# Performance work log

Measured on AMD Instinct MI355X. Metric: run time of the kernel, lower is better.

## Reference

```python
import jax, jax.numpy as jnp
import numpy as np
from jax import lax

B, C, H, W = 16, 512, 32, 32
CQ = C // 16


def _conv(x, w, b):
    # NCHW input, OIHW kernel, 3x3 stride-1 'SAME' == torch padding=1
    o = lax.conv_general_dilated(x, w, (1, 1), 'SAME',
                                 dimension_numbers=('NCHW', 'OIHW', 'NCHW'))
    return o + b[None, :, None, None]


def setup_inputs() -> dict:
    key = jax.random.key(0)
    ks = jax.random.split(key, 8)
    fan_q = C * 9
    fan_v = C * 9
    return {
        'x': jax.random.normal(ks[0], (B, C, H, W), jnp.float32),
        'y': jax.random.normal(ks[1], (B, C, H, W), jnp.float32),
        'wq': jax.random.normal(ks[2], (CQ, C, 3, 3), jnp.float32) / np.sqrt(fan_q),
        'bq': jnp.zeros((CQ,), jnp.float32),
        'wk': jax.random.normal(ks[3], (CQ, C, 3, 3), jnp.float32) / np.sqrt(fan_q),
        'bk': jnp.zeros((CQ,), jnp.float32),
        'wv': jax.random.normal(ks[4], (C, C, 3, 3), jnp.float32) / np.sqrt(fan_v),
        'bv': jnp.zeros((C,), jnp.float32),
    }


def reference(x, y, wq, bq, wk, bk, wv, bv):
    b, c, h, w = x.shape
    n = h * w
    q = _conv(x, wq, bq).reshape(b, -1, n)   # (B, CQ, N)
    k = _conv(y, wk, bk).reshape(b, -1, n)   # (B, CQ, N)
    v = _conv(y, wv, bv).reshape(b, c, n)    # (B, C, N)
    # energy[b, i, j] = <q[:, i], k[:, j]>  (unscaled, non-causal)
    energy = jnp.einsum('bdi,bdj->bij', q, k)           # (B, N, N)
    attn = jax.nn.softmax(energy, axis=-1)              # softmax over keys j
    # out[b, c, i] = sum_j v[b, c, j] * attn[b, i, j]
    out = jnp.einsum('bcj,bij->bci', v, attn)           # (B, C, N)
    return out.reshape(b, c, h, w)
```

## Files before the change

kernel.cpp:

```cpp
#include <hip/hip_runtime.h>

#define BB 16
#define CCH 512
#define CQD 32
#define HH 32
#define WW 32
#define NN 1024
#define PH 34

typedef __attribute__((ext_vector_type(8))) _Float16 half8;
typedef __attribute__((ext_vector_type(4))) _Float16 half4;
typedef __attribute__((ext_vector_type(4))) float f32x4;

static __device__ __forceinline__ void gload_lds16(const void* g, void* l) {
    __builtin_amdgcn_global_load_lds(
        (const __attribute__((address_space(1))) unsigned int*)g,
        (__attribute__((address_space(3))) unsigned int*)l, 16, 0, 0);
}

__global__ __launch_bounds__(256) void prep_all_kernel(
    const float* __restrict__ x, const float* __restrict__ y,
    const float* __restrict__ wv, const float* __restrict__ wq,
    const float* __restrict__ wk,
    _Float16* __restrict__ xp, _Float16* __restrict__ yp,
    _Float16* __restrict__ wvh, _Float16* __restrict__ wqkh)
{
    const int bid = blockIdx.x;
    const int t = threadIdx.x;

    if (bid >= 1088) {
        const int wb = bid - 1088;
        const float* src;
        _Float16* dst;
        int co_src, co_dst;
        if (wb < 512)      { src = wv; co_src = wb;       dst = wvh;  co_dst = wb; }
        else if (wb < 544) { src = wq; co_src = wb - 512; dst = wqkh; co_dst = wb - 512; }
        else               { src = wk; co_src = wb - 544; dst = wqkh; co_dst = 32 + (wb - 544); }
        for (int idx = t; idx < 4608; idx += 256) {
            int tap = idx / 512, ci = idx - tap * 512;
            dst[(size_t)co_dst * 4608 + idx] = (_Float16)src[(size_t)co_src * 4608 + ci * 9 + tap];
        }
        return;
    }

    const int h = bid >> 5;
    const int which = (bid >> 4) & 1, b = bid & 15;
    const float* img = which ? y : x;
    _Float16* row = (which ? yp : xp) + (size_t)(b * PH + h) * PH * CCH;
    const int gh = h - 1;

    half8 z;
    #pragma unroll
    for (int u = 0; u < 8; ++u) z[u] = (_Float16)0.f;

    if (gh < 0 || gh >= HH) {
        for (int idx = t; idx < PH * CCH / 8; idx += 256)
            *(half8*)&row[(size_t)idx * 8] = z;
        return;
    }

    __shared__ float X[64][33];
    for (int ci0 = 0; ci0 < CCH; ci0 += 64) {
        __syncthreads();
        #pragma unroll
        for (int i = 0; i < 8; ++i) {
            int ci = i * 8 + (t >> 5), w = t & 31;
            X[ci][w] = img[((size_t)(b * CCH + ci0 + ci) * HH + gh) * WW + w];
        }
        __syncthreads();
        int w = t >> 3, g = t & 7;
        half8 o;
        #pragma unroll
        for (int u = 0; u < 8; ++u) o[u] = (_Float16)X[g * 8 + u][w];
        *(half8*)&row[(size_t)(w + 1) * CCH + ci0 + g * 8] = o;
        if (t < 16) {
            int col = (t < 8) ? 0 : 33;
            *(half8*)&row[(size_t)col * CCH + ci0 + (t & 7) * 8] = z;
        }
    }
}

__global__ __launch_bounds__(256, 2) void conv_v_mfma_kernel(
    const _Float16* __restrict__ yp,
    const _Float16* __restrict__ wvh,
    const float* __restrict__ bvb,
    _Float16* __restrict__ vout)
{
    const int pt  = blockIdx.x;
    const int co0 = blockIdx.y * 64;
    const int b   = blockIdx.z;

    __shared__ __align__(16) _Float16 Wl[64 * 296];
    __shared__ __align__(16) _Float16 Yl[13824];

    const int t    = threadIdx.x;
    const int lane = t & 63;
    const int wv4  = t >> 6;
    const int l15  = lane & 15;
    const int kg   = lane >> 4;

    f32x4 acc[4][4];
    #pragma unroll
    for (int m = 0; m < 4; ++m)
        #pragma unroll
        for (int n = 0; n < 4; ++n) {
            f32x4 z = {0.f, 0.f, 0.f, 0.f};
            acc[m][n] = z;
        }

    const int r0p = pt * 8;
    int bbase[4];
    #pragma unroll
    for (int n = 0; n < 4; ++n) {
        int pxl = wv4 * 64 + n * 16 + l15;
        int rl = pxl >> 5, cl = pxl & 31;
        bbase[n] = (rl * 34 + cl) * 40 + kg * 8;
    }
    int abase[4];
    #pragma unroll
    for (int m = 0; m < 4; ++m)
        abase[m] = (m * 16 + l15) * 296 + kg * 8;

    #pragma unroll 1
    for (int ci0 = 0; ci0 < CCH; ci0 += 32) {
        __syncthreads();
        #pragma unroll
        for (int i = 0; i < 10; ++i) {
            int d = t + i * 256;
            if (d < 2368) {
                int c = d / 37, rem = d - c * 37;
                const _Float16* g = (rem < 36)
                    ? &wvh[(size_t)(co0 + c) * 4608 + (rem >> 2) * 512 + ci0 + (rem & 3) * 8]
                    : wvh;
                gload_lds16(g, (char*)Wl + (size_t)(i * 256 + wv4 * 64) * 16);
            }
        }
        #pragma unroll
        for (int i = 0; i < 7; ++i) {
            int d = t + i * 256;
            if (d < 1728) {
                int rc = d / 5, part = d - rc * 5;
                const _Float16* g = yp;
                if (rc < 340 && part < 4) {
                    int r = rc / 34, c = rc - r * 34;
                    g = &yp[((size_t)(b * PH + r0p + r) * PH + c) * CCH + ci0 + part * 8];
                }
                gload_lds16(g, (char*)Yl + (size_t)(i * 256 + wv4 * 64) * 16);
            }
        }
        __syncthreads();

        #pragma unroll
        for (int tap = 0; tap < 9; ++tap) {
            const int dh = tap / 3, dw = tap % 3;
            half8 a[4], bf[4];
            #pragma unroll
            for (int m = 0; m < 4; ++m)
                a[m] = *(const half8*)&Wl[abase[m] + tap * 32];
            #pragma unroll
            for (int n = 0; n < 4; ++n)
                bf[n] = *(const half8*)&Yl[bbase[n] + (dh * 34 + dw) * 40];
            #pragma unroll
            for (int m = 0; m < 4; ++m)
                #pragma unroll
                for (int n = 0; n < 4; ++n)
                    acc[m][n] = __builtin_amdgcn_mfma_f32_16x16x32_f16(a[m], bf[n], acc[m][n], 0, 0, 0);
        }
    }

    #pragma unroll
    for (int m = 0; m < 4; ++m) {
        #pragma unroll
        for (int reg = 0; reg < 4; ++reg) {
            int co = co0 + m * 16 + kg * 4 + reg;
            float bias = bvb[co];
            #pragma unroll
            for (int n = 0; n < 4; ++n) {
                int px = pt * 256 + wv4 * 64 + n * 16 + l15;
                vout[((size_t)b * CCH + co) * NN + px] = (_Float16)(acc[m][n][reg] + bias);
            }
        }
    }
}

__global__ __launch_bounds__(256, 4) void conv_qk_split_kernel(
    const _Float16* __restrict__ xp,
    const _Float16* __restrict__ yp,
    const _Float16* __restrict__ wqkh,
    float* __restrict__ pbuf)
{
    const int pt    = blockIdx.x >> 2;
    const int ks    = blockIdx.x & 3;
    const int which = blockIdx.y;
    const int b     = blockIdx.z;
    const _Float16* in = which ? yp : xp;

    __shared__ __align__(16) _Float16 Wl[9728];
    __shared__ __align__(16) _Float16 Xl[8192];

    const int t    = threadIdx.x;
    const int lane = t & 63;
    const int w    = t >> 6;
    const int l15  = lane & 15;
    const int kg   = lane >> 4;

    f32x4 acc[2][2];
    #pragma unroll
    for (int m = 0; m < 2; ++m)
        #pragma unroll
        for (int n = 0; n < 2; ++n) {
            f32x4 z = {0.f, 0.f, 0.f, 0.f};
            acc[m][n] = z;
        }

    const int r0p = pt * 4;
    int bbase[2];
    #pragma unroll
    for (int n = 0; n < 2; ++n) {
        int pxl = w * 32 + n * 16 + l15;
        int rl = pxl >> 5, cl = pxl & 31;
        bbase[n] = (rl * 34 + cl) * 40 + kg * 8;
    }
    int abase[2];
    #pragma unroll
    for (int m = 0; m < 2; ++m)
        abase[m] = (m * 16 + l15) * 296 + kg * 8;

    #pragma unroll 1
    for (int cc = 0; cc < 4; ++cc) {
        const int ci0 = ks * 128 + cc * 32;
        __syncthreads();
        #pragma unroll
        for (int i = 0; i < 5; ++i) {
            int d = t + i * 256;
            if (d < 1216) {
                const _Float16* g = wqkh;
                if (d < 1184) {
                    int c = d / 37, rem = d - c * 37;
                    if (rem < 36)
                        g = &wqkh[(size_t)(which * 32 + c) * 4608 + (rem >> 2) * 512 + ci0 + (rem & 3) * 8];
                }
                gload_lds16(g, (char*)Wl + (size_t)(i * 256 + w * 64) * 16);
            }
        }
        #pragma unroll
        for (int i = 0; i < 4; ++i) {
            int d = t + i * 256;
            int rc = d / 5, part = d - rc * 5;
            const _Float16* g = in;
            if (rc < 204 && part < 4) {
                int r = rc / 34, c = rc - r * 34;
                g = &in[((size_t)(b * PH + r0p + r) * PH + c) * CCH + ci0 + part * 8];
            }
            gload_lds16(g, (char*)Xl + (size_t)(i * 256 + w * 64) * 16);
        }
        __syncthreads();

        #pragma unroll
        for (int tap = 0; tap < 9; ++tap) {
            const int dh = tap / 3, dw = tap % 3;
            half8 a[2], bfr[2];
            #pragma unroll
            for (int m = 0; m < 2; ++m)
                a[m] = *(const half8*)&Wl[abase[m] + tap * 32];
            #pragma unroll
            for (int n = 0; n < 2; ++n)
                bfr[n] = *(const half8*)&Xl[bbase[n] + (dh * 34 + dw) * 40];
            #pragma unroll
            for (int m = 0; m < 2; ++m)
                #pragma unroll
                for (int n = 0; n < 2; ++n)
                    acc[m][n] = __builtin_amdgcn_mfma_f32_16x16x32_f16(a[m], bfr[n], acc[m][n], 0, 0, 0);
        }
    }

    float* pb = &pbuf[(((size_t)(ks * 2 + which) * BB + b) * NN) * CQD];
    #pragma unroll
    for (int n = 0; n < 2; ++n) {
        int px = pt * 128 + w * 32 + n * 16 + l15;
        #pragma unroll
        for (int m = 0; m < 2; ++m) {
            float4 o = make_float4(acc[m][n][0], acc[m][n][1], acc[m][n][2], acc[m][n][3]);
            *(float4*)&pb[(size_t)px * CQD + m * 16 + kg * 4] = o;
        }
    }
}

__global__ __launch_bounds__(256) void qk_reduce_kernel(
    const float* __restrict__ pbuf,
    const float* __restrict__ bq, const float* __restrict__ bk,
    _Float16* __restrict__ qh, _Float16* __restrict__ kh)
{
    const int gid   = blockIdx.x * 256 + threadIdx.x;
    const int cog   = gid & 7;
    const int px    = (gid >> 3) & 1023;
    const int b     = (gid >> 13) & 15;
    const int which = gid >> 17;

    const size_t base = (((size_t)which * BB + b) * NN + px) * CQD + cog * 4;
    const size_t kstep = (size_t)2 * BB * NN * CQD;
    float4 s = *(const float4*)&pbuf[base];
    #pragma unroll
    for (int ks = 1; ks < 4; ++ks) {
        float4 p = *(const float4*)&pbuf[base + ks * kstep];
        s.x += p.x; s.y += p.y; s.z += p.z; s.w += p.w;
    }
    const float* bias = which ? bk : bq;
    float4 bv = *(const float4*)&bias[cog * 4];
    half4 o;
    o[0] = (_Float16)(s.x + bv.x);
    o[1] = (_Float16)(s.y + bv.y);
    o[2] = (_Float16)(s.z + bv.z);
    o[3] = (_Float16)(s.w + bv.w);
    _Float16* out = which ? kh : qh;
    *(half4*)&out[((size_t)b * NN + px) * CQD + cog * 4] = o;
}

__global__ __launch_bounds__(256, 2) void attn_fused_kernel(
    const _Float16* __restrict__ qh,
    const _Float16* __restrict__ kh,
    const _Float16* __restrict__ v,
    float* __restrict__ out)
{
    const int wg   = blockIdx.x;
    const int virt = (wg & 7) * 64 + (wg >> 3);
    const int b    = virt >> 5;
    const int i0   = (virt & 31) * 32;

    __shared__ __align__(16) _Float16 Pl[32 * 136];
    float* redm = (float*)Pl;
    float* redl = redm + 32 * 17;

    const int t    = threadIdx.x;
    const int lane = t & 63;
    const int w    = t >> 6;
    const int l15  = lane & 15;
    const int kg   = lane >> 4;

    half8 qb[2];
    #pragma unroll
    for (int n = 0; n < 2; ++n)
        qb[n] = *(const half8*)&qh[((size_t)b * NN + i0 + n * 16 + l15) * CQD + kg * 8];

    float m[2] = {-3.0e38f, -3.0e38f}, l[2] = {0.f, 0.f};
    #pragma unroll 1
    for (int jp = 0; jp < 8; ++jp) {
        #pragma unroll
        for (int ht = 0; ht < 2; ++ht) {
            int j = jp * 128 + ht * 64 + w * 16 + l15;
            half8 ak = *(const half8*)&kh[((size_t)b * NN + j) * CQD + kg * 8];
            #pragma unroll
            for (int n = 0; n < 2; ++n) {
                f32x4 s = {0.f, 0.f, 0.f, 0.f};
                s = __builtin_amdgcn_mfma_f32_16x16x32_f16(ak, qb[n], s, 0, 0, 0);
                float tm = fmaxf(fmaxf(s[0], s[1]), fmaxf(s[2], s[3]));
                float m2 = fmaxf(m[n], tm);
                l[n] = l[n] * __expf(m[n] - m2)
                     + __expf(s[0] - m2) + __expf(s[1] - m2)
                     + __expf(s[2] - m2) + __expf(s[3] - m2);
                m[n] = m2;
            }
        }
    }
    #pragma unroll
    for (int n = 0; n < 2; ++n) {
        redm[(n * 16 + l15) * 17 + w * 4 + kg] = m[n];
        redl[(n * 16 + l15) * 17 + w * 4 + kg] = l[n];
    }
    __syncthreads();
    float mr[2], rl[2];
    #pragma unroll
    for (int n = 0; n < 2; ++n) {
        const int i = n * 16 + l15;
        float M = redm[i * 17];
        #pragma unroll
        for (int p = 1; p < 16; ++p) M = fmaxf(M, redm[i * 17 + p]);
        float L = 0.f;
        #pragma unroll
        for (int p = 0; p < 16; ++p) L += redl[i * 17 + p] * __expf(redm[i * 17 + p] - M);
        mr[n] = M;
        rl[n] = 1.f / L;
    }

    f32x4 acc[4][2][2];
    #pragma unroll
    for (int cc = 0; cc < 4; ++cc)
        #pragma unroll
        for (int mm = 0; mm < 2; ++mm)
            #pragma unroll
            for (int n = 0; n < 2; ++n) {
                f32x4 z = {0.f, 0.f, 0.f, 0.f};
                acc[cc][mm][n] = z;
            }

    #pragma unroll 1
    for (int jp = 0; jp < 8; ++jp) {
        __syncthreads();
        #pragma unroll
        for (int ht = 0; ht < 2; ++ht) {
            int j = jp * 128 + ht * 64 + w * 16 + l15;
            half8 ak = *(const half8*)&kh[((size_t)b * NN + j) * CQD + kg * 8];
            #pragma unroll
            for (int n = 0; n < 2; ++n) {
                f32x4 s = {0.f, 0.f, 0.f, 0.f};
                s = __builtin_amdgcn_mfma_f32_16x16x32_f16(ak, qb[n], s, 0, 0, 0);
                half4 p4;
                #pragma unroll
                for (int reg = 0; reg < 4; ++reg)
                    p4[reg] = (_Float16)(__expf(s[reg] - mr[n]) * rl[n]);
                *(half4*)&Pl[(n * 16 + l15) * 136 + ht * 64 + w * 16 + kg * 4] = p4;
            }
        }
        __syncthreads();
        #pragma unroll
        for (int cc = 0; cc < 4; ++cc) {
            #pragma unroll
            for (int ks = 0; ks < 4; ++ks) {
                half8 pb[2], va[2];
                #pragma unroll
                for (int n = 0; n < 2; ++n)
                    pb[n] = *(const half8*)&Pl[(n * 16 + l15) * 136 + ks * 32 + kg * 8];
                #pragma unroll
                for (int mm = 0; mm < 2; ++mm) {
                    int c = cc * 128 + w * 32 + mm * 16 + l15;
                    va[mm] = *(const half8*)&v[((size_t)b * CCH + c) * NN + jp * 128 + ks * 32 + kg * 8];
                }
                #pragma unroll
                for (int mm = 0; mm < 2; ++mm)
                    #pragma unroll
                    for (int n = 0; n < 2; ++n)
                        acc[cc][mm][n] = __builtin_amdgcn_mfma_f32_16x16x32_f16(va[mm], pb[n], acc[cc][mm][n], 0, 0, 0);
            }
        }
    }

    #pragma unroll
    for (int cc = 0; cc < 4; ++cc)
        #pragma unroll
        for (int mm = 0; mm < 2; ++mm)
            #pragma unroll
            for (int n = 0; n < 2; ++n)
                #pragma unroll
                for (int reg = 0; reg < 4; ++reg) {
                    int c = cc * 128 + w * 32 + mm * 16 + kg * 4 + reg;
                    out[((size_t)b * CCH + c) * NN + i0 + n * 16 + l15] = acc[cc][mm][n][reg];
                }
}

extern "C" void kernel_launch(void* const* d_in, const int* in_sizes, int n_in,
                              void* d_out, int out_size, void* d_ws, size_t ws_size,
                              hipStream_t stream) {
    const float* x  = (const float*)d_in[0];
    const float* y  = (const float*)d_in[1];
    const float* wq = (const float*)d_in[2];
    const float* bq = (const float*)d_in[3];
    const float* wk = (const float*)d_in[4];
    const float* bk = (const float*)d_in[5];
    const float* wv = (const float*)d_in[6];
    const float* bv = (const float*)d_in[7];
    float* out = (float*)d_out;

    _Float16* qhb = (_Float16*)d_ws;
    _Float16* khb = qhb + (size_t)BB * NN * CQD;
    _Float16* vb   = khb + (size_t)BB * NN * CQD;
    _Float16* ypb  = vb + (size_t)BB * CCH * NN;
    _Float16* xpb  = ypb + (size_t)BB * PH * PH * CCH;
    _Float16* wvh  = xpb + (size_t)BB * PH * PH * CCH;
    _Float16* wqkh = wvh + (size_t)512 * 4608;
    float* pbuf = (float*)vb;

    prep_all_kernel<<<dim3(1088 + 576), 256, 0, stream>>>(x, y, wv, wq, wk, xpb, ypb, wvh, wqkh);
    conv_qk_split_kernel<<<dim3(32, 2, BB), 256, 0, stream>>>(xpb, ypb, wqkh, pbuf);
    qk_reduce_kernel<<<dim3(1024), 256, 0, stream>>>(pbuf, bq, bk, qhb, khb);
    conv_v_mfma_kernel<<<dim3(4, 8, BB), 256, 0, stream>>>(ypb, wvh, bv, vb);
    attn_fused_kernel<<<dim3(512), 256, 0, stream>>>(qhb, khb, vb, out);
}
```

Measured before the change: 201.7 us.

## Retile attention to 64 queries x 256 channels and stage V tiles in LDS

```diff
diff --git a/kernel.cpp b/kernel.cpp
--- a/kernel.cpp
+++ b/kernel.cpp
@@ -325,11 +325,14 @@
     const int wg   = blockIdx.x;
     const int virt = (wg & 7) * 64 + (wg >> 3);
     const int b    = virt >> 5;
-    const int i0   = (virt & 31) * 32;
-
-    __shared__ __align__(16) _Float16 Pl[32 * 136];
+    const int rem5 = virt & 31;
+    const int c0   = (rem5 >> 4) * 256;
+    const int i0   = (rem5 & 15) * 64;
+
+    __shared__ __align__(16) _Float16 Vl[2][64 * 136];
+    __shared__ __align__(16) _Float16 Pl[64 * 136];
     float* redm = (float*)Pl;
-    float* redl = redm + 32 * 17;
+    float* redl = redm + 64 * 17;
 
     const int t    = threadIdx.x;
     const int lane = t & 63;
@@ -337,12 +340,28 @@
     const int l15  = lane & 15;
     const int kg   = lane >> 4;
 
-    half8 qb[2];
-    #pragma unroll
-    for (int n = 0; n < 2; ++n)
+    #define STAGE_V(dst, jp_, cc_)                                              \
+        {                                                                       \
+            _Pragma("unroll")                                                   \
+            for (int i_ = 0; i_ < 5; ++i_) {                                    \
+                int d_ = t + i_ * 256;                                          \
+                if (d_ < 1088) {                  \
+                    int r_ = d_ / 17, rem_ = d_ - r_ * 17;                      \
+                    const _Float16* g_ = (rem_ < 16)                            \
+                        ? &v[((size_t)b * CCH + c0 + (cc_) * 64 + r_) * NN + (jp_) * 128 + rem_ * 8] \
+                        : v;                                                    \
+                    gload_lds16(g_, (char*)(dst) + (size_t)(i_ * 256 + w * 64) * 16); \
+                }                                                               \
+            }                                                                   \
+        }
+
+    half8 qb[4];
+    #pragma unroll
+    for (int n = 0; n < 4; ++n)
         qb[n] = *(const half8*)&qh[((size_t)b * NN + i0 + n * 16 + l15) * CQD + kg * 8];
 
-    float m[2] = {-3.0e38f, -3.0e38f}, l[2] = {0.f, 0.f};
+    float m[4] = {-3.0e38f, -3.0e38f, -3.0e38f, -3.0e38f};
+    float l[4] = {0.f, 0.f, 0.f, 0.f};
     #pragma unroll 1
     for (int jp = 0; jp < 8; ++jp) {
         #pragma unroll
@@ -350,7 +369,7 @@
             int j = jp * 128 + ht * 64 + w * 16 + l15;
             half8 ak = *(const half8*)&kh[((size_t)b * NN + j) * CQD + kg * 8];
             #pragma unroll
-            for (int n = 0; n < 2; ++n) {
+            for (int n = 0; n < 4; ++n) {
                 f32x4 s = {0.f, 0.f, 0.f, 0.f};
                 s = __builtin_amdgcn_mfma_f32_16x16x32_f16(ak, qb[n], s, 0, 0, 0);
                 float tm = fmaxf(fmaxf(s[0], s[1]), fmaxf(s[2], s[3]));
@@ -363,14 +382,14 @@
         }
     }
     #pragma unroll
-    for (int n = 0; n < 2; ++n) {
+    for (int n = 0; n < 4; ++n) {
         redm[(n * 16 + l15) * 17 + w * 4 + kg] = m[n];
         redl[(n * 16 + l15) * 17 + w * 4 + kg] = l[n];
     }
     __syncthreads();
-    float mr[2], rl[2];
-    #pragma unroll
-    for (int n = 0; n < 2; ++n) {
+    float mr[4], rl[4];
+    #pragma unroll
+    for (int n = 0; n < 4; ++n) {
         const int i = n * 16 + l15;
         float M = redm[i * 17];
         #pragma unroll
@@ -382,26 +401,25 @@
         rl[n] = 1.f / L;
     }
 
-    f32x4 acc[4][2][2];
+    f32x4 acc[4][4];
     #pragma unroll
     for (int cc = 0; cc < 4; ++cc)
         #pragma unroll
-        for (int mm = 0; mm < 2; ++mm)
-            #pragma unroll
-            for (int n = 0; n < 2; ++n) {
-                f32x4 z = {0.f, 0.f, 0.f, 0.f};
-                acc[cc][mm][n] = z;
-            }
+        for (int n = 0; n < 4; ++n) {
+            f32x4 z = {0.f, 0.f, 0.f, 0.f};
+            acc[cc][n] = z;
+        }
 
     #pragma unroll 1
     for (int jp = 0; jp < 8; ++jp) {
         __syncthreads();
+        STAGE_V(Vl[0], jp, 0);
         #pragma unroll
         for (int ht = 0; ht < 2; ++ht) {
             int j = jp * 128 + ht * 64 + w * 16 + l15;
             half8 ak = *(const half8*)&kh[((size_t)b * NN + j) * CQD + kg * 8];
             #pragma unroll
-            for (int n = 0; n < 2; ++n) {
+            for (int n = 0; n < 4; ++n) {
                 f32x4 s = {0.f, 0.f, 0.f, 0.f};
                 s = __builtin_amdgcn_mfma_f32_16x16x32_f16(ak, qb[n], s, 0, 0, 0);
                 half4 p4;
@@ -411,25 +429,22 @@
                 *(half4*)&Pl[(n * 16 + l15) * 136 + ht * 64 + w * 16 + kg * 4] = p4;
             }
         }
-        __syncthreads();
         #pragma unroll
         for (int cc = 0; cc < 4; ++cc) {
+            __syncthreads();
+            if (cc < 3) {
+                _Float16* vnxt = (_Float16*)Vl[(cc + 1) & 1];
+                STAGE_V(vnxt, jp, cc + 1);
+            }
+            const _Float16* vcur = (const _Float16*)Vl[cc & 1];
             #pragma unroll
             for (int ks = 0; ks < 4; ++ks) {
-                half8 pb[2], va[2];
+                half8 va = *(const half8*)&vcur[(w * 16 + l15) * 136 + ks * 32 + kg * 8];
                 #pragma unroll
-                for (int n = 0; n < 2; ++n)
-                    pb[n] = *(const half8*)&Pl[(n * 16 + l15) * 136 + ks * 32 + kg * 8];
-                #pragma unroll
-                for (int mm = 0; mm < 2; ++mm) {
-                    int c = cc * 128 + w * 32 + mm * 16 + l15;
-                    va[mm] = *(const half8*)&v[((size_t)b * CCH + c) * NN + jp * 128 + ks * 32 + kg * 8];
+                for (int n = 0; n < 4; ++n) {
+                    half8 pb = *(const half8*)&Pl[(n * 16 + l15) * 136 + ks * 32 + kg * 8];
+                    acc[cc][n] = __builtin_amdgcn_mfma_f32_16x16x32_f16(va, pb, acc[cc][n], 0, 0, 0);
                 }
-                #pragma unroll
-                for (int mm = 0; mm < 2; ++mm)
-                    #pragma unroll
-                    for (int n = 0; n < 2; ++n)
-                        acc[cc][mm][n] = __builtin_amdgcn_mfma_f32_16x16x32_f16(va[mm], pb[n], acc[cc][mm][n], 0, 0, 0);
             }
         }
     }
@@ -437,14 +452,13 @@
     #pragma unroll
     for (int cc = 0; cc < 4; ++cc)
         #pragma unroll
-        for (int mm = 0; mm < 2; ++mm)
-            #pragma unroll
-            for (int n = 0; n < 2; ++n)
-                #pragma unroll
-                for (int reg = 0; reg < 4; ++reg) {
-                    int c = cc * 128 + w * 32 + mm * 16 + kg * 4 + reg;
-                    out[((size_t)b * CCH + c) * NN + i0 + n * 16 + l15] = acc[cc][mm][n][reg];
-                }
+        for (int n = 0; n < 4; ++n)
+            #pragma unroll
+            for (int reg = 0; reg < 4; ++reg) {
+                int c = c0 + cc * 64 + w * 16 + kg * 4 + reg;
+                out[((size_t)b * CCH + c) * NN + i0 + n * 16 + l15] = acc[cc][n][reg];
+            }
+    #undef STAGE_V
 }
 
 extern "C" void kernel_launch(void* const* d_in, const int* in_sizes, int n_in,
```

After: 170.5 us (median of 2 runs). 1.18x faster.
